# Optimization experiments

Measured on AMD Instinct MI355X. Metric: run time of the kernel, lower is better.

Reference implementation:

```python
import jax, jax.numpy as jnp
import numpy as np

B, L, D, H = 2, 4096, 512, 8
HD = D // H
SCALE = 1.0 / (D / H) ** 0.5


def setup_inputs() -> dict:
    key = jax.random.key(0)
    ks = jax.random.split(key, 12)
    s = 0.02
    inp = {
        "q": jax.random.normal(ks[0], (B, L, D), jnp.float32),
        "k": jax.random.normal(ks[1], (B, L, D), jnp.float32),
        "v": jax.random.normal(ks[2], (B, L, D), jnp.float32),
        # causal mask, True = keep (masked_fill where mask == False)
        "mask": jnp.tril(jnp.ones((L, L), bool))[None, None, :, :],
        "Wq": jax.random.normal(ks[3], (D, D), jnp.float32) * s,
        "bq": jnp.zeros((D,), jnp.float32),
        "Wk": jax.random.normal(ks[4], (D, D), jnp.float32) * s,
        "bk": jnp.zeros((D,), jnp.float32),
        "Wv": jax.random.normal(ks[5], (D, D), jnp.float32) * s,
        "bv": jnp.zeros((D,), jnp.float32),
        "Wo": jax.random.normal(ks[6], (D, D), jnp.float32) * s,
        "bo": jnp.zeros((D,), jnp.float32),
    }
    return inp


def _split_heads(x):
    # [B, L, D] -> [B, H, L, HD]
    b, l, d = x.shape
    return x.reshape(b, l, H, HD).transpose(0, 2, 1, 3)


def reference(q, k, v, mask, Wq, bq, Wk, bk, Wv, bv, Wo, bo):
    # Dropout is inference-mode (identity), matching module.eval().
    qh = _split_heads(q @ Wq.T + bq)          # [B,H,L,HD]
    kh = _split_heads(k @ Wk.T + bk)          # [B,H,L,HD]
    vh = _split_heads(v @ Wv.T + bv)          # [B,H,L,HD]
    scores = jnp.einsum("bhqd,bhkd->bhqk", qh, kh) * SCALE
    scores = jnp.where(mask, scores, -jnp.inf)
    attn = jax.nn.softmax(scores, axis=-1)
    out = jnp.einsum("bhqk,bhkd->bhqd", attn, vh)  # [B,H,L,HD]
    out = out.transpose(0, 2, 1, 3).reshape(q.shape[0], q.shape[1], D)
    return out @ Wo.T + bo
```

## Files before the change

### kernel.cpp

```cpp
#include <hip/hip_runtime.h>

typedef __bf16 bf16;
typedef __bf16 bf16x4 __attribute__((ext_vector_type(4)));
typedef __bf16 bf16x8 __attribute__((ext_vector_type(8)));
typedef float  f32x4  __attribute__((ext_vector_type(4)));
typedef float  f32x16 __attribute__((ext_vector_type(16)));

#define NB   2
#define NL   4096
#define ND   512
#define NH   8
#define NHD  64

static __device__ __forceinline__ void g2l16(const bf16* g, bf16* l) {
    __builtin_amdgcn_global_load_lds(
        (const __attribute__((address_space(1))) unsigned int*)g,
        (__attribute__((address_space(3))) unsigned int*)l, 16, 0, 0);
}

__global__ __launch_bounds__(256) void cvt_all(
    const float* __restrict__ q, const float* __restrict__ k, const float* __restrict__ v,
    const float* __restrict__ Wq, const float* __restrict__ Wk,
    const float* __restrict__ Wv, const float* __restrict__ Wo,
    bf16* __restrict__ qb, bf16* __restrict__ kb, bf16* __restrict__ vb,
    bf16* __restrict__ wqb, bf16* __restrict__ wkb,
    bf16* __restrict__ wvb, bf16* __restrict__ wob)
{
    const int z = blockIdx.z;
    const float* src; bf16* dst; int n4;
    switch (z) {
        case 0: src = q;  dst = qb;  n4 = NB * NL * ND / 4; break;
        case 1: src = k;  dst = kb;  n4 = NB * NL * ND / 4; break;
        case 2: src = v;  dst = vb;  n4 = NB * NL * ND / 4; break;
        case 3: src = Wq; dst = wqb; n4 = ND * ND / 4; break;
        case 4: src = Wk; dst = wkb; n4 = ND * ND / 4; break;
        case 5: src = Wv; dst = wvb; n4 = ND * ND / 4; break;
        default: src = Wo; dst = wob; n4 = ND * ND / 4; break;
    }
    for (int i = blockIdx.x * 256 + threadIdx.x; i < n4; i += gridDim.x * 256) {
        const f32x4 a = *(const f32x4*)(src + (size_t)i * 4);
        bf16x4 o;
        #pragma unroll
        for (int j = 0; j < 4; ++j) o[j] = (bf16)a[j];
        *(bf16x4*)(dst + (size_t)i * 4) = o;
    }
}

__global__ __launch_bounds__(256) void proj_qkv(
    const bf16* __restrict__ qb, const bf16* __restrict__ kb, const bf16* __restrict__ vb,
    const bf16* __restrict__ wq, const bf16* __restrict__ wk, const bf16* __restrict__ wv,
    const float* __restrict__ biasq, const float* __restrict__ biask, const float* __restrict__ biasv,
    bf16* __restrict__ qh, bf16* __restrict__ kh, bf16* __restrict__ vt)
{
    const int z = blockIdx.z;
    const bf16* X     = (z == 0) ? qb : (z == 1) ? kb : vb;
    const bf16* W     = (z == 0) ? wq : (z == 1) ? wk : wv;
    const float* bias = (z == 0) ? biasq : (z == 1) ? biask : biasv;

    const int m0 = blockIdx.y * 128;
    const int n0 = blockIdx.x * 128;

    __shared__ bf16 As[2][128 * 32];
    __shared__ bf16 Bs[2][128 * 32];

    const int t    = threadIdx.x;
    const int lane = t & 63;
    const int wm   = (t >> 7) & 1;
    const int wn   = (t >> 6) & 1;
    const int quad = lane >> 4;
    const int l16  = lane & 15;

    auto stage = [&](int k0, int buf) {
        #pragma unroll
        for (int p = 0; p < 2; ++p) {
            const int id = p * 256 + t;
            const int r = id >> 2, s = id & 3;
            const int c = (s ^ (r & 3)) * 8;
            g2l16(X + (size_t)(m0 + r) * ND + k0 + c, As[buf] + id * 8);
            g2l16(W + (size_t)(n0 + r) * ND + k0 + c, Bs[buf] + id * 8);
        }
    };

    f32x4 acc[4][4] = {};
    stage(0, 0);

    for (int it = 0; it < 16; ++it) {
        __syncthreads();
        if (it + 1 < 16) stage((it + 1) * 32, (it + 1) & 1);

        const bf16* as = As[it & 1];
        const bf16* bs = Bs[it & 1];
        bf16x8 aF[4], bF[4];
        #pragma unroll
        for (int i = 0; i < 4; ++i) {
            const int ra = wm * 64 + i * 16 + l16;
            const int rb = wn * 64 + i * 16 + l16;
            aF[i] = *(const bf16x8*)(as + ra * 32 + (quad ^ (ra & 3)) * 8);
            bF[i] = *(const bf16x8*)(bs + rb * 32 + (quad ^ (rb & 3)) * 8);
        }
        #pragma unroll
        for (int mt = 0; mt < 4; ++mt)
            #pragma unroll
            for (int nt = 0; nt < 4; ++nt)
                acc[mt][nt] = __builtin_amdgcn_mfma_f32_16x16x32_bf16(
                    aF[mt], bF[nt], acc[mt][nt], 0, 0, 0);
    }

    const float oscale = (z == 0) ? 0.125f : (z == 1) ? 1.4426950408889634f : 1.0f;
    #pragma unroll
    for (int nt = 0; nt < 4; ++nt) {
        const int col = n0 + wn * 64 + nt * 16 + l16;
        const float bb = bias[col];
        const int h = col >> 6, hd = col & 63;
        #pragma unroll
        for (int mt = 0; mt < 4; ++mt) {
            const int row0 = m0 + wm * 64 + mt * 16 + quad * 4;
            const int b = row0 >> 12;
            const int l = row0 & 4095;
            if (z == 2) {
                bf16x4 val;
                #pragma unroll
                for (int r = 0; r < 4; ++r) val[r] = (bf16)(acc[mt][nt][r] + bb);
                *(bf16x4*)(vt + ((size_t)(b * NH + h) * NHD + hd) * NL + l) = val;
            } else {
                bf16* dst = (z == 0) ? qh : kh;
                #pragma unroll
                for (int r = 0; r < 4; ++r)
                    dst[((size_t)(b * NH + h) * NL + (l + r)) * NHD + hd] =
                        (bf16)((acc[mt][nt][r] + bb) * oscale);
            }
        }
    }
}

#define PW 72
__global__ __launch_bounds__(512, 2) void attn(
    const bf16* __restrict__ qh, const bf16* __restrict__ kh,
    const bf16* __restrict__ vt, bf16* __restrict__ ao)
{
    const int bh  = blockIdx.x;
    const int b   = bh >> 3, h = bh & 7;
    const int qtA = blockIdx.y;
    const int qtB = 31 - qtA;
    const int nA  = 2 * qtA + 2;
    const int nB  = 2 * qtB + 2;

    __shared__ bf16 smem[32768 + 8 * 32 * PW];

    const int t    = threadIdx.x;
    const int wave = t >> 6;
    const int g    = wave >> 2;
    const int w4   = wave & 3;
    const int lane = t & 63;
    const int l32  = lane & 31;
    const int half = lane >> 5;
    const int sb   = g * 16384;
    const int tg   = t & 255;

    const bf16* Qg = qh + (size_t)bh * NL * NHD;
    const bf16* Kg = kh + (size_t)bh * NL * NHD;
    const bf16* Vg = vt + (size_t)bh * NHD * NL;

    #pragma unroll
    for (int p = 0; p < 4; ++p) {
        const int id = p * 512 + t;
        const int tile = id >> 10, r = (id >> 3) & 127, s = id & 7;
        const int q0 = (tile ? qtB : qtA) * 128;
        g2l16(Qg + (size_t)(q0 + r) * NHD + s * 8, smem + id * 8);
    }
    __syncthreads();

    bf16x8 qfA[4], qfB[4];
    #pragma unroll
    for (int c = 0; c < 4; ++c) {
        qfA[c] = *(const bf16x8*)(smem +        (w4 * 32 + l32) * 64 + c * 16 + half * 8);
        qfB[c] = *(const bf16x8*)(smem + 8192 + (w4 * 32 + l32) * 64 + c * 16 + half * 8);
    }
    __syncthreads();

    auto stage_kv = [&](int k0, int buf) {
        #pragma unroll
        for (int p = 0; p < 2; ++p) {
            const int id = p * 256 + tg;
            const int r = id >> 3, s = id & 7;
            g2l16(Kg + (size_t)(k0 + r) * NHD + ((s ^ (r & 7)) * 8),
                  smem + sb + buf * 8192 + id * 8);
            g2l16(Vg + (size_t)r * NL + k0 + ((s ^ (r & 7)) * 8),
                  smem + sb + buf * 8192 + 4096 + id * 8);
        }
    };
    stage_kv(0, 0);

    f32x16 o_acc[2] = {};
    float l_lane = 0.f;

    for (int jj = 0; jj < 33; ++jj) {
        __syncthreads();

        if (jj + 1 < 33) {
            const int jn = jj + 1;
            const int kvn = (g == 0) ? jn : (jn < nA ? jn : jn - nA + 33);
            stage_kv(kvn * 64, jn & 1);
        }

        if (g == 1 && jj == nA) {
            const float lt = l_lane + __shfl_xor(l_lane, 32, 64);
            const float rcp = 1.0f / fmaxf(lt, 1e-20f);
            const int row = qtA * 128 + w4 * 32 + l32;
            #pragma unroll
            for (int mt2 = 0; mt2 < 2; ++mt2)
                #pragma unroll
                for (int rr = 0; rr < 4; ++rr) {
                    const int hd = mt2 * 32 + rr * 8 + half * 4;
                    bf16x4 val;
                    #pragma unroll
                    for (int rb = 0; rb < 4; ++rb)
                        val[rb] = (bf16)(o_acc[mt2][rr * 4 + rb] * rcp);
                    *(bf16x4*)(ao + ((size_t)b * NL + row) * ND + h * NHD + hd) = val;
                }
            o_acc[0] = (f32x16)(0.f); o_acc[1] = (f32x16)(0.f);
            l_lane = 0.f;
        }

        const bool useA  = (g == 1) && (jj < nA);
        const int j_glob = (g == 0) ? jj : (useA ? jj : jj - nA + 33);
        const int qt_cur = useA ? qtA : qtB;

        const bf16* ks = smem + sb + (jj & 1) * 8192;
        const bf16* vs = ks + 4096;

        f32x16 sacc[2] = {};
        #pragma unroll
        for (int c = 0; c < 4; ++c) {
            const bf16x8 qf = useA ? qfA[c] : qfB[c];
            #pragma unroll
            for (int mt = 0; mt < 2; ++mt) {
                const int row   = mt * 32 + l32;
                const int chunk = 2 * c + half;
                const bf16x8 kf = *(const bf16x8*)(ks + row * 64 + ((chunk ^ (row & 7)) * 8));
                sacc[mt] = __builtin_amdgcn_mfma_f32_32x32x16_bf16(
                    kf, qf, sacc[mt], 0, 0, 0);
            }
        }

        const bool diag = (j_glob >= 2 * qt_cur);
        const int  dq   = j_glob * 64 - qt_cur * 128;
        const int  qrow_l = w4 * 32 + l32;
        bf16* pw = smem + 32768 + wave * 32 * PW;
        #pragma unroll
        for (int mt = 0; mt < 2; ++mt) {
            #pragma unroll
            for (int rr = 0; rr < 4; ++rr) {
                const int kvb = mt * 32 + rr * 8 + half * 4;
                bf16x4 val;
                #pragma unroll
                for (int rb = 0; rb < 4; ++rb) {
                    float e;
                    if (diag && (dq + kvb + rb > qrow_l)) e = 0.f;
                    else e = exp2f(sacc[mt][rr * 4 + rb]);
                    l_lane += e;
                    val[rb] = (bf16)e;
                }
                *(bf16x4*)(pw + l32 * PW + kvb) = val;
            }
        }

        #pragma unroll
        for (int c = 0; c < 4; ++c) {
            const bf16x8 pf = *(const bf16x8*)(pw + l32 * PW + c * 16 + half * 8);
            #pragma unroll
            for (int mt2 = 0; mt2 < 2; ++mt2) {
                const int row = mt2 * 32 + l32;
                const int u8  = 2 * c + half;
                const bf16x8 vf = *(const bf16x8*)(vs + row * 64 + ((u8 ^ (row & 7)) * 8));
                o_acc[mt2] = __builtin_amdgcn_mfma_f32_32x32x16_bf16(
                    vf, pf, o_acc[mt2], 0, 0, 0);
            }
        }
    }

    __syncthreads();
    float* comb = (float*)smem;
    if (g == 1) {
        const int base = w4 * (64 * 36) + lane * 36;
        #pragma unroll
        for (int mt2 = 0; mt2 < 2; ++mt2)
            #pragma unroll
            for (int i = 0; i < 16; ++i)
                comb[base + mt2 * 16 + i] = o_acc[mt2][i];
        const float lt = l_lane + __shfl_xor(l_lane, 32, 64);
        if (half == 0) comb[9216 + w4 * 32 + l32] = lt;
    }
    __syncthreads();
    if (g == 0) {
        const int base = w4 * (64 * 36) + lane * 36;
        const float lt = l_lane + __shfl_xor(l_lane, 32, 64)
                       + comb[9216 + w4 * 32 + l32];
        const float rcp = 1.0f / fmaxf(lt, 1e-20f);
        const int row = qtB * 128 + w4 * 32 + l32;
        #pragma unroll
        for (int mt2 = 0; mt2 < 2; ++mt2)
            #pragma unroll
            for (int rr = 0; rr < 4; ++rr) {
                const int hd = mt2 * 32 + rr * 8 + half * 4;
                bf16x4 val;
                #pragma unroll
                for (int rb = 0; rb < 4; ++rb)
                    val[rb] = (bf16)((o_acc[mt2][rr * 4 + rb] +
                                      comb[base + mt2 * 16 + rr * 4 + rb]) * rcp);
                *(bf16x4*)(ao + ((size_t)b * NL + row) * ND + h * NHD + hd) = val;
            }
    }
}

__global__ __launch_bounds__(256) void out_proj(
    const bf16* __restrict__ ao, const bf16* __restrict__ wo,
    const float* __restrict__ bo, float* __restrict__ out)
{
    const int m0 = blockIdx.y * 128;
    const int n0 = blockIdx.x * 128;

    __shared__ bf16 As[2][128 * 32];
    __shared__ bf16 Bs[2][128 * 32];

    const int t    = threadIdx.x;
    const int lane = t & 63;
    const int wm   = (t >> 7) & 1;
    const int wn   = (t >> 6) & 1;
    const int quad = lane >> 4;
    const int l16  = lane & 15;

    auto stage = [&](int k0, int buf) {
        #pragma unroll
        for (int p = 0; p < 2; ++p) {
            const int id = p * 256 + t;
            const int r = id >> 2, s = id & 3;
            const int c = (s ^ (r & 3)) * 8;
            g2l16(ao + (size_t)(m0 + r) * ND + k0 + c, As[buf] + id * 8);
            g2l16(wo + (size_t)(n0 + r) * ND + k0 + c, Bs[buf] + id * 8);
        }
    };

    f32x4 acc[4][4] = {};
    stage(0, 0);

    for (int it = 0; it < 16; ++it) {
        __syncthreads();
        if (it + 1 < 16) stage((it + 1) * 32, (it + 1) & 1);

        const bf16* as = As[it & 1];
        const bf16* bs = Bs[it & 1];
        bf16x8 aF[4], bF[4];
        #pragma unroll
        for (int i = 0; i < 4; ++i) {
            const int ra = wm * 64 + i * 16 + l16;
            const int rb = wn * 64 + i * 16 + l16;
            aF[i] = *(const bf16x8*)(as + ra * 32 + (quad ^ (ra & 3)) * 8);
            bF[i] = *(const bf16x8*)(bs + rb * 32 + (quad ^ (rb & 3)) * 8);
        }
        #pragma unroll
        for (int mt = 0; mt < 4; ++mt)
            #pragma unroll
            for (int nt = 0; nt < 4; ++nt)
                acc[mt][nt] = __builtin_amdgcn_mfma_f32_16x16x32_bf16(
                    aF[mt], bF[nt], acc[mt][nt], 0, 0, 0);
    }

    #pragma unroll
    for (int nt = 0; nt < 4; ++nt) {
        const int col = n0 + wn * 64 + nt * 16 + l16;
        const float bb = bo[col];
        #pragma unroll
        for (int mt = 0; mt < 4; ++mt) {
            const int row0 = m0 + wm * 64 + mt * 16 + quad * 4;
            #pragma unroll
            for (int r = 0; r < 4; ++r)
                out[(size_t)(row0 + r) * ND + col] = acc[mt][nt][r] + bb;
        }
    }
}

extern "C" void kernel_launch(void* const* d_in, const int* in_sizes, int n_in,
                              void* d_out, int out_size, void* d_ws, size_t ws_size,
                              hipStream_t stream) {
    (void)in_sizes; (void)n_in; (void)out_size; (void)ws_size;

    const float* q  = (const float*)d_in[0];
    const float* k  = (const float*)d_in[1];
    const float* v  = (const float*)d_in[2];
    const float* Wq = (const float*)d_in[4];
    const float* bq = (const float*)d_in[5];
    const float* Wk = (const float*)d_in[6];
    const float* bk = (const float*)d_in[7];
    const float* Wv = (const float*)d_in[8];
    const float* bv = (const float*)d_in[9];
    const float* Wo = (const float*)d_in[10];
    const float* bo = (const float*)d_in[11];

    const size_t XSZ = (size_t)NB * NL * ND;
    const size_t WSZ = (size_t)ND * ND;
    bf16* p = (bf16*)d_ws;
    bf16* qb  = p; p += XSZ;
    bf16* kb  = p; p += XSZ;
    bf16* vb  = p; p += XSZ;
    bf16* wqb = p; p += WSZ;
    bf16* wkb = p; p += WSZ;
    bf16* wvb = p; p += WSZ;
    bf16* wob = p; p += WSZ;
    bf16* qh  = p; p += XSZ;
    bf16* kh  = p; p += XSZ;
    bf16* vt  = p; p += XSZ;
    bf16* ao  = p; p += XSZ;

    cvt_all<<<dim3(512, 1, 7), 256, 0, stream>>>(
        q, k, v, Wq, Wk, Wv, Wo, qb, kb, vb, wqb, wkb, wvb, wob);

    dim3 g1(ND / 128, (NB * NL) / 128, 3);
    proj_qkv<<<g1, 256, 0, stream>>>(qb, kb, vb, wqb, wkb, wvb, bq, bk, bv, qh, kh, vt);

    dim3 g2(16, 16, 1);
    attn<<<g2, 512, 0, stream>>>(qh, kh, vt, ao);

    dim3 g3(ND / 128, (NB * NL) / 128, 1);
    out_proj<<<g3, 256, 0, stream>>>(ao, wob, bo, (float*)d_out);
}
```

Measured before the change: 261.0 us.

## Keep softmax probabilities in registers via permlane32 swap instead of LDS round-trip

Rebuilds the P operand for the PV MFMA directly from the score accumulators. It packs them with v_cvt_pk_bf16_f32 and exchanges halves across lanes with permlane32_swap, so the per-wave LDS scratch buffer and its write/read round trip go away. Each wave now holds only one Q fragment set, and group-1 waves reload the B tile's Q from global memory when they switch tiles. This cuts LDS use and register pressure but adds a global load mid-loop and depends on the permlane lane mapping being correct.

```diff
diff --git a/kernel.cpp b/kernel.cpp
--- a/kernel.cpp
+++ b/kernel.cpp
@@ -5,6 +5,8 @@
 typedef __bf16 bf16x8 __attribute__((ext_vector_type(8)));
 typedef float  f32x4  __attribute__((ext_vector_type(4)));
 typedef float  f32x16 __attribute__((ext_vector_type(16)));
+typedef unsigned int u32x2 __attribute__((ext_vector_type(2)));
+typedef unsigned int u32x4 __attribute__((ext_vector_type(4)));
 
 #define NB   2
 #define NL   4096
@@ -133,7 +135,6 @@
     }
 }
 
-#define PW 72
 __global__ __launch_bounds__(512, 2) void attn(
     const bf16* __restrict__ qh, const bf16* __restrict__ kh,
     const bf16* __restrict__ vt, bf16* __restrict__ ao)
@@ -143,9 +144,8 @@
     const int qtA = blockIdx.y;
     const int qtB = 31 - qtA;
     const int nA  = 2 * qtA + 2;
-    const int nB  = 2 * qtB + 2;
-
-    __shared__ bf16 smem[32768 + 8 * 32 * PW];
+
+    __shared__ bf16 smem[32768];
 
     const int t    = threadIdx.x;
     const int wave = t >> 6;
@@ -170,11 +170,12 @@
     }
     __syncthreads();
 
-    bf16x8 qfA[4], qfB[4];
-    #pragma unroll
-    for (int c = 0; c < 4; ++c) {
-        qfA[c] = *(const bf16x8*)(smem +        (w4 * 32 + l32) * 64 + c * 16 + half * 8);
-        qfB[c] = *(const bf16x8*)(smem + 8192 + (w4 * 32 + l32) * 64 + c * 16 + half * 8);
+    bf16x8 qf[4];
+    {
+        const int qoff = (g == 0) ? 8192 : 0;
+        #pragma unroll
+        for (int c = 0; c < 4; ++c)
+            qf[c] = *(const bf16x8*)(smem + qoff + (w4 * 32 + l32) * 64 + c * 16 + half * 8);
     }
     __syncthreads();
 
@@ -220,6 +221,10 @@
                 }
             o_acc[0] = (f32x16)(0.f); o_acc[1] = (f32x16)(0.f);
             l_lane = 0.f;
+            const bf16* Qt = Qg + (size_t)(qtB * 128 + w4 * 32 + l32) * NHD;
+            #pragma unroll
+            for (int c = 0; c < 4; ++c)
+                qf[c] = *(const bf16x8*)(Qt + c * 16 + half * 8);
         }
 
         const bool useA  = (g == 1) && (jj < nA);
@@ -232,42 +237,50 @@
         f32x16 sacc[2] = {};
         #pragma unroll
         for (int c = 0; c < 4; ++c) {
-            const bf16x8 qf = useA ? qfA[c] : qfB[c];
             #pragma unroll
             for (int mt = 0; mt < 2; ++mt) {
                 const int row   = mt * 32 + l32;
                 const int chunk = 2 * c + half;
                 const bf16x8 kf = *(const bf16x8*)(ks + row * 64 + ((chunk ^ (row & 7)) * 8));
                 sacc[mt] = __builtin_amdgcn_mfma_f32_32x32x16_bf16(
-                    kf, qf, sacc[mt], 0, 0, 0);
+                    kf, qf[c], sacc[mt], 0, 0, 0);
             }
         }
 
-        const bool diag = (j_glob >= 2 * qt_cur);
-        const int  dq   = j_glob * 64 - qt_cur * 128;
+        const bool diag   = (j_glob >= 2 * qt_cur);
+        const int  dq     = j_glob * 64 - qt_cur * 128;
         const int  qrow_l = w4 * 32 + l32;
-        bf16* pw = smem + 32768 + wave * 32 * PW;
         #pragma unroll
         for (int mt = 0; mt < 2; ++mt) {
             #pragma unroll
-            for (int rr = 0; rr < 4; ++rr) {
-                const int kvb = mt * 32 + rr * 8 + half * 4;
-                bf16x4 val;
-                #pragma unroll
-                for (int rb = 0; rb < 4; ++rb) {
-                    float e;
-                    if (diag && (dq + kvb + rb > qrow_l)) e = 0.f;
-                    else e = exp2f(sacc[mt][rr * 4 + rb]);
-                    l_lane += e;
-                    val[rb] = (bf16)e;
-                }
-                *(bf16x4*)(pw + l32 * PW + kvb) = val;
+            for (int r = 0; r < 16; ++r) {
+                const int kv = mt * 32 + (r & 3) + 8 * (r >> 2) + 4 * half;
+                float e;
+                if (diag && (dq + kv > qrow_l)) e = 0.f;
+                else e = exp2f(sacc[mt][r]);
+                l_lane += e;
+                sacc[mt][r] = e;
             }
         }
 
         #pragma unroll
         for (int c = 0; c < 4; ++c) {
-            const bf16x8 pf = *(const bf16x8*)(pw + l32 * PW + c * 16 + half * 8);
+            const int mt = c >> 1;
+            const int b0 = (c & 1) * 8;
+            unsigned w0, w1, w2, w3;
+            asm("v_cvt_pk_bf16_f32 %0, %1, %2" : "=v"(w0)
+                : "v"(sacc[mt][b0 + 0]), "v"(sacc[mt][b0 + 1]));
+            asm("v_cvt_pk_bf16_f32 %0, %1, %2" : "=v"(w1)
+                : "v"(sacc[mt][b0 + 2]), "v"(sacc[mt][b0 + 3]));
+            asm("v_cvt_pk_bf16_f32 %0, %1, %2" : "=v"(w2)
+                : "v"(sacc[mt][b0 + 4]), "v"(sacc[mt][b0 + 5]));
+            asm("v_cvt_pk_bf16_f32 %0, %1, %2" : "=v"(w3)
+                : "v"(sacc[mt][b0 + 6]), "v"(sacc[mt][b0 + 7]));
+            const u32x2 s02 = __builtin_amdgcn_permlane32_swap(w0, w2, false, false);
+            const u32x2 s13 = __builtin_amdgcn_permlane32_swap(w1, w3, false, false);
+            u32x4 pw_ = { s02.x, s13.x, s02.y, s13.y };
+            bf16x8 pf;
+            __builtin_memcpy(&pf, &pw_, 16);
             #pragma unroll
             for (int mt2 = 0; mt2 < 2; ++mt2) {
                 const int row = mt2 * 32 + l32;
```

New measurement: 260.2 us. Within noise of the previous version (-0.3%).
